# Kernel optimization log

Hardware: AMD Instinct MI355X
Metric: run time of the kernel (lower is better)

Reference implementation:

```python
import jax, jax.numpy as jnp
import numpy as np
from jax import lax

# program token ids
PAD, START, END, SCENE, INTERSECT, FILT, RELATE, QUERY = range(8)
SKIP = (PAD, START, END)


def conv2d(x, w, b, dil=1):
    # 'same' padding for odd kernels (3x3 pad=dil, 1x1 pad=0), NCHW/OIHW
    pad = dil * (w.shape[2] // 2)
    y = lax.conv_general_dilated(x, w, (1, 1), [(pad, pad), (pad, pad)],
                                 rhs_dilation=(dil, dil),
                                 dimension_numbers=('NCHW', 'OIHW', 'NCHW'))
    return y + b[None, :, None, None]


def maxpool2(x):
    return lax.reduce_window(x, -jnp.inf, lax.max, (1, 1, 2, 2), (1, 1, 2, 2), 'VALID')


def exec_program(prog, feat_input, p):
    """Run one (concrete) program over a batch of stem features. prog: tuple of ints,
    executed in reversed order exactly like TbDNet.forward."""
    B, _, H, W = feat_input.shape
    output = feat_input
    saved = None
    for t in reversed(prog):
        if t in SKIP:
            continue
        if t == SCENE:
            saved = output
            output = jnp.ones((B, 1, H, W), feat_input.dtype)
        elif t == INTERSECT:  # AndModule: elementwise min of attentions
            output = jnp.minimum(output, saved)
        elif t == FILT:
            a = feat_input * output  # [B,D,H,W] * [B,1,H,W]
            a = jax.nn.relu(conv2d(a, p['att_w1'], p['att_b1']))
            a = jax.nn.relu(conv2d(a, p['att_w2'], p['att_b2']))
            output = jax.nn.sigmoid(conv2d(a, p['att_w3'], p['att_b3']))
        elif t == RELATE:  # RelateModule: dilated conv stack (1,2,4,8,1) -> conv1x1 sigmoid
            a = feat_input * output
            for w, b, d in ((p['rel_w1'], p['rel_b1'], 1), (p['rel_w2'], p['rel_b2'], 2),
                            (p['rel_w3'], p['rel_b3'], 4), (p['rel_w4'], p['rel_b4'], 8),
                            (p['rel_w5'], p['rel_b5'], 1)):
                a = jax.nn.relu(conv2d(a, w, b, d))
            output = jax.nn.sigmoid(conv2d(a, p['rel_w6'], p['rel_b6']))
        elif t == QUERY:
            a = feat_input * output
            a = jax.nn.relu(conv2d(a, p['qry_w1'], p['qry_b1']))
            output = jax.nn.relu(conv2d(a, p['qry_w2'], p['qry_b2']))
    return output


def tbd_forward(feats, programs_np, p):
    B = feats.shape[0]
    stem = jax.nn.relu(conv2d(feats, p['stem_w1'], p['stem_b1']))
    stem = jax.nn.relu(conv2d(stem, p['stem_w2'], p['stem_b2']))  # [B,D,H,W]
    D, H, W = stem.shape[1], stem.shape[2], stem.shape[3]
    # group samples by identical program so dispatch runs batched, not per-sample
    groups = {}
    for n in range(B):
        groups.setdefault(tuple(int(v) for v in programs_np[n]), []).append(n)
    mod_out = jnp.zeros((B, D, H, W), feats.dtype)
    for prog, idxs in groups.items():
        idx = jnp.array(idxs)
        mod_out = mod_out.at[idx].set(exec_program(prog, stem[idx], p))
    # classifier: conv1x1 -> relu -> maxpool2 -> flatten -> fc -> relu -> fc
    x = jax.nn.relu(conv2d(mod_out, p['cls_w'], p['cls_b']))
    x = maxpool2(x)                        # [B,1024,7,7]
    x = x.reshape(B, -1)                   # [B,50176]
    x = jax.nn.relu(x @ p['fc1_w'].T + p['fc1_b'])
    return x @ p['fc2_w'].T + p['fc2_b']   # [B,28]


def setup_inputs() -> dict:
    key = jax.random.key(0)
    ks = iter(jax.random.split(key, 64))
    def rn(shape, s=0.05):
        return jax.random.normal(next(ks), shape, dtype=jnp.float32) * s
    B, Cin, H, W, D, P, L, A = 64, 1024, 14, 14, 128, 1024, 1024, 28
    feats = jax.random.normal(next(ks), (B, Cin, H, W), dtype=jnp.float32)
    # stored programs; execution order is reversed(stored)
    progA = [START, QUERY, FILT, RELATE, FILT, SCENE, END, PAD]            # scene->filter->relate->filter->query
    progB = [START, QUERY, INTERSECT, FILT, SCENE, FILT, SCENE, END]       # two filter branches -> intersect -> query
    programs = jnp.array([progA] * (B // 2) + [progB] * (B // 2), dtype=jnp.int32)
    inp = {'feats': feats, 'programs': programs,
           'stem_w1': rn((D, Cin, 3, 3), 0.02), 'stem_b1': rn((D,)),
           'stem_w2': rn((D, D, 3, 3)), 'stem_b2': rn((D,)),
           'att_w1': rn((D, D, 3, 3)), 'att_b1': rn((D,)),
           'att_w2': rn((D, D, 3, 3)), 'att_b2': rn((D,)),
           'att_w3': rn((1, D, 1, 1)), 'att_b3': rn((1,)),
           'rel_w1': rn((D, D, 3, 3)), 'rel_b1': rn((D,)),
           'rel_w2': rn((D, D, 3, 3)), 'rel_b2': rn((D,)),
           'rel_w3': rn((D, D, 3, 3)), 'rel_b3': rn((D,)),
           'rel_w4': rn((D, D, 3, 3)), 'rel_b4': rn((D,)),
           'rel_w5': rn((D, D, 3, 3)), 'rel_b5': rn((D,)),
           'rel_w6': rn((1, D, 1, 1)), 'rel_b6': rn((1,)),
           'qry_w1': rn((D, D, 3, 3)), 'qry_b1': rn((D,)),
           'qry_w2': rn((D, D, 3, 3)), 'qry_b2': rn((D,)),
           'cls_w': rn((P, D, 1, 1)), 'cls_b': rn((P,)),
           'fc1_w': rn((L, P * (H // 2) * (W // 2)), 0.01), 'fc1_b': rn((L,)),
           'fc2_w': rn((A, L)), 'fc2_b': rn((A,))}
    return inp


PARAM_NAMES = ['stem_w1', 'stem_b1', 'stem_w2', 'stem_b2',
               'att_w1', 'att_b1', 'att_w2', 'att_b2', 'att_w3', 'att_b3',
               'rel_w1', 'rel_b1', 'rel_w2', 'rel_b2', 'rel_w3', 'rel_b3',
               'rel_w4', 'rel_b4', 'rel_w5', 'rel_b5', 'rel_w6', 'rel_b6',
               'qry_w1', 'qry_b1', 'qry_w2', 'qry_b2',
               'cls_w', 'cls_b', 'fc1_w', 'fc1_b', 'fc2_w', 'fc2_b']


def reference(feats, programs, stem_w1, stem_b1, stem_w2, stem_b2,
              att_w1, att_b1, att_w2, att_b2, att_w3, att_b3,
              rel_w1, rel_b1, rel_w2, rel_b2, rel_w3, rel_b3,
              rel_w4, rel_b4, rel_w5, rel_b5, rel_w6, rel_b6,
              qry_w1, qry_b1, qry_w2, qry_b2,
              cls_w, cls_b, fc1_w, fc1_b, fc2_w, fc2_b):
    vals = [stem_w1, stem_b1, stem_w2, stem_b2,
            att_w1, att_b1, att_w2, att_b2, att_w3, att_b3,
            rel_w1, rel_b1, rel_w2, rel_b2, rel_w3, rel_b3,
            rel_w4, rel_b4, rel_w5, rel_b5, rel_w6, rel_b6,
            qry_w1, qry_b1, qry_w2, qry_b2,
            cls_w, cls_b, fc1_w, fc1_b, fc2_w, fc2_b]
    p = dict(zip(PARAM_NAMES, vals))
    return tbd_forward(feats, np.asarray(programs), p)
```

## Files before the change

kernel.cpp:

```cpp
#include <hip/hip_runtime.h>
#include <math.h>


typedef __attribute__((ext_vector_type(8)))  short   short8;
typedef __attribute__((ext_vector_type(8)))  __bf16  bf16x8;
typedef __attribute__((ext_vector_type(4)))  float   f32x4;

#define NROUNDS 11
#define NKS 98
#define S1KS 16

#define B_WSTEM1 0UL
#define B_WSTEM2 2359296UL
#define B_WMOD   2654208UL
#define B_WCLS   5308416UL
#define B_STEM   5570560UL
#define B_XA     8781824UL
#define B_XB     11993088UL
#define B_FEAT   15204352UL
#define B_ATTN   18415616UL
#define B_SAVED  18465792UL
#define B_SCHED  18515968UL
#define B_ACTB   18520064UL
#define B_FC1T   24942592UL
#define B_P1X1   25204736UL
#define B_S1P    67108864UL
#define B_FC1P   134217728UL

__device__ __forceinline__ unsigned short f2bf(float f) {
    __bf16 h = (__bf16)f;
    union { __bf16 h; unsigned short u; } c; c.h = h; return c.u;
}
__device__ __forceinline__ float bf2f(unsigned short u) {
    return __uint_as_float(((unsigned int)u) << 16);
}
__device__ __forceinline__ unsigned int pkbf(float a, float b) {
    return (unsigned int)f2bf(a) | ((unsigned int)f2bf(b) << 16);
}
__device__ __forceinline__ f32x4 mfma16(bf16x8 a, bf16x8 b, f32x4 c) {
    return __builtin_amdgcn_mfma_f32_16x16x32_bf16(a, b, c, 0, 0, 0);
}

struct PrepArgs { const float* src[12]; const int* prog; char* ws; };

__global__ __launch_bounds__(256) void k_prep(PrepArgs a)
{
    char* ws = a.ws;
    const int bx = blockIdx.x;
    if (bx < 768) {
        const int y = bx >> 6;
        const float* __restrict__ src = a.src[y];
        int gid = (bx & 63) * 256 + threadIdx.x;
        int gsz = 64 * 256;
        if (y == 11) {
            unsigned short* dst = (unsigned short*)(ws + B_WCLS);
            for (int i = gid; i < 131072; i += gsz) dst[i] = f2bf(src[i]);
        } else {
            const int IC = (y == 0) ? 1024 : 128;
            const int lg = (y == 0) ? 10 : 7;
            unsigned short* dst = (unsigned short*)(ws + ((y == 0) ? B_WSTEM1
                                        : (y == 1) ? B_WSTEM2
                                        : B_WMOD + (size_t)(y - 2) * 294912));
            const int total = 9 << (lg + 7);
            for (int i = gid; i < total; i += gsz) {
                int ic = i & (IC - 1);
                int oc = (i >> lg) & 127;
                int t  = i >> (lg + 7);
                dst[i] = f2bf(src[((size_t)oc * IC + ic) * 9 + t]);
            }
        }
        return;
    }
    int gid = (bx - 768) * 256 + threadIdx.x;
    int gsz = 256 * 256;
    float* attn  = (float*)(ws + B_ATTN);
    float* saved = (float*)(ws + B_SAVED);
    float* p1    = (float*)(ws + B_P1X1);
    for (int i = gid; i < 64 * 196; i += gsz) { attn[i] = 1.0f; saved[i] = 1.0f; }
    for (int i = gid; i < 8 * 64 * 196; i += gsz) p1[i] = 0.0f;
    unsigned int* fz = (unsigned int*)(ws + B_FEAT);
    for (int i = gid; i < 64 * 25088 / 2; i += gsz) fz[i] = 0u;
    if (gid < 64) {
        int n = gid;
        const int* prog = a.prog;
        int ent[NROUNDS];
        for (int r = 0; r < NROUNDS; ++r) ent[r] = 0;
        int rc = 0, nslot = 0;
        int pscene = 0, pinter = 0, pmat = 0, pmw = 0;
#define PREBITS ((pscene<<17)|(pinter<<18)|(pmat<<19)|(pmw<<22))
#define CLRPRE  (pscene = pinter = pmat = pmw = 0)
#define EMIT(v) do { if (rc < NROUNDS) ent[rc++] = (v); } while (0)
        for (int j = 7; j >= 0; --j) {
            int t = prog[n * 8 + j];
            switch (t) {
                case 3: pscene = 1; break;
                case 4: pinter = 1; break;
                case 5: {
                    int e1 = 3 | (0<<4) | (1<<8) | (1<<12) | (2<<13) | (0<<15) | PREBITS;
                    CLRPRE; EMIT(e1);
                    EMIT(3 | (1<<4) | (1<<8) | (0<<12) | (0<<13) | (1<<15)
                           | (1<<23) | (0<<24) | (nslot<<25));
                    pmat = nslot + 1; pmw = 0; nslot++;
                    break;
                }
                case 6: {
                    int e1 = 3 | (2<<4) | (1<<8) | (1<<12) | (2<<13) | (0<<15) | PREBITS;
                    CLRPRE; EMIT(e1);
                    EMIT(3 | (3<<4) | (2<<8) | (0<<12) | (0<<13) | (1<<15));
                    EMIT(3 | (4<<4) | (4<<8) | (0<<12) | (1<<13) | (0<<15));
                    EMIT(3 | (5<<4) | (8<<8) | (0<<12) | (0<<13) | (1<<15));
                    EMIT(3 | (6<<4) | (1<<8) | (0<<12) | (1<<13) | (0<<15)
                           | (1<<23) | (1<<24) | (nslot<<25));
                    pmat = nslot + 1; pmw = 1; nslot++;
                    break;
                }
                case 7: {
                    int e1 = 3 | (7<<4) | (1<<8) | (1<<12) | (2<<13) | (0<<15) | PREBITS;
                    CLRPRE; EMIT(e1);
                    EMIT(3 | (8<<4) | (1<<8) | (0<<12) | (0<<13) | (2<<15));
                    break;
                }
                default: break;
            }
        }
#undef EMIT
#undef PREBITS
#undef CLRPRE
        int* sched = (int*)(ws + B_SCHED);
        for (int r = 0; r < NROUNDS; ++r) sched[n * NROUNDS + r] = ent[r];
    }
}

__global__ __launch_bounds__(512) void k_stem1p(const float* __restrict__ feats,
                                                const unsigned short* __restrict__ wrep,
                                                char* ws)
{
    __shared__ unsigned short s_img[197 * 72];
    const int bx = blockIdx.x;
    const int n = bx >> 4, ks = bx & 15;
    const int tid = threadIdx.x, lane = tid & 63;
    const int w = tid >> 6, wm = w & 1, wn = w >> 1;
    const int l15 = lane & 15, lq = lane >> 4;

    if (tid < 36) ((unsigned int*)(s_img + 196 * 72))[tid] = 0u;

    int pglob[4], pbyt[4], pyv[4], pxv[4];
#pragma unroll
    for (int j = 0; j < 4; ++j) {
        int p  = (wn + 4 * j) * 16 + l15;
        pglob[j] = p;
        int py = p / 14;
        pyv[j] = (p < 196) ? py : 10000;
        pxv[j] = p - py * 14;
        pbyt[j] = p * 144 + lq * 16;
    }
    const int zaddr = 196 * 144 + lq * 16;
    const int nJ = (wn == 0) ? 4 : 3;

    f32x4 acc[4][4];
#pragma unroll
    for (int m = 0; m < 4; ++m)
#pragma unroll
        for (int j = 0; j < 4; ++j) acc[m][j] = (f32x4){0.f, 0.f, 0.f, 0.f};

    const int icg = tid & 15;
    const int qq0 = tid >> 4;
    const int icb = ks * 64;

    const float* sf = feats + ((size_t)n * 1024 + icb) * 196;
    for (int qq = qq0; qq < 49; qq += 32) {
        const float* p0 = sf + icg * 4 * 196 + qq * 4;
        float4 r0 = *(const float4*)(p0);
        float4 r1 = *(const float4*)(p0 + 196);
        float4 r2 = *(const float4*)(p0 + 392);
        float4 r3 = *(const float4*)(p0 + 588);
#pragma unroll
        for (int e = 0; e < 4; ++e) {
            uint2 v;
            v.x = pkbf(((const float*)&r0)[e], ((const float*)&r1)[e]);
            v.y = pkbf(((const float*)&r2)[e], ((const float*)&r3)[e]);
            *(uint2*)(s_img + (qq * 4 + e) * 72 + icg * 4) = v;
        }
    }
    __syncthreads();

#pragma unroll
    for (int t = 0; t < 9; ++t) {
        const int dy = t / 3 - 1, dx = t % 3 - 1;
        int baddr[4];
#pragma unroll
        for (int j = 0; j < 4; ++j) {
            int yy = pyv[j] + dy, xx = pxv[j] + dx;
            bool ok = ((unsigned)yy < 14u) && ((unsigned)xx < 14u);
            baddr[j] = ok ? (pbyt[j] + (dy * 14 + dx) * 144) : zaddr;
        }
#pragma unroll
        for (int kc = 0; kc < 2; ++kc) {
            const unsigned short* wt = wrep +
                ((size_t)(t * 128 + wm * 64 + l15) * 1024 + icb + kc * 32 + lq * 8);
            bf16x8 am[4];
#pragma unroll
            for (int m = 0; m < 4; ++m)
                am[m] = *(const bf16x8*)(wt + (size_t)m * 16 * 1024);
#pragma unroll
            for (int j = 0; j < 4; ++j) {
                if (j < nJ) {
                    bf16x8 b = *(const bf16x8*)((const char*)s_img + baddr[j] + kc * 64);
#pragma unroll
                    for (int m = 0; m < 4; ++m)
                        acc[m][j] = mfma16(am[m], b, acc[m][j]);
                }
            }
        }
    }

    unsigned short* part = (unsigned short*)(ws + B_S1P);
#pragma unroll
    for (int m = 0; m < 4; ++m) {
        const int oc = wm * 64 + m * 16 + lq * 4;
#pragma unroll
        for (int j = 0; j < 4; ++j) {
            if (j < nJ) {
                int p = pglob[j];
                if (p < 196) {
                    uint2 pk;
                    pk.x = pkbf(acc[m][j][0], acc[m][j][1]);
                    pk.y = pkbf(acc[m][j][2], acc[m][j][3]);
                    *(uint2*)(part + (((size_t)ks * 64 + n) * 196 + p) * 128 + oc) = pk;
                }
            }
        }
    }
}

__global__ __launch_bounds__(256) void k_stem1r(const char* __restrict__ ws_c,
                                                const float* __restrict__ bias,
                                                unsigned short* __restrict__ xa)
{
    int i = blockIdx.x * 256 + threadIdx.x;
    const unsigned short* part = (const unsigned short*)(ws_c + B_S1P);
    int oc8 = (i & 15) * 8;
    int np  = i >> 4;
    float s[8] = {};
#pragma unroll
    for (int ks = 0; ks < S1KS; ++ks) {
        short8 v = *(const short8*)(part + (((size_t)ks * 64) * 196 + np) * 128 + oc8);
#pragma unroll
        for (int e = 0; e < 8; ++e) s[e] += bf2f((unsigned short)v[e]);
    }
    short8 o;
#pragma unroll
    for (int e = 0; e < 8; ++e)
        o[e] = (short)f2bf(fmaxf(s[e] + bias[oc8 + e], 0.f));
    *(short8*)(xa + (size_t)np * 128 + oc8) = o;
}

__device__ void conv_core32(const unsigned short* __restrict__ srcB,
                            const float* __restrict__ s_gate,
                            const unsigned short* __restrict__ wrep,
                            const float* __restrict__ bias,
                            unsigned short* __restrict__ dst,
                            int dil, int oct, int pxh,
                            unsigned short* s_img,
                            int post, const float* __restrict__ pwv,
                            float* __restrict__ pdst)
{
    const int tid  = threadIdx.x, lane = tid & 63;
    const int w    = tid >> 6, wm = w & 1, wn = w >> 1;
    const int l15  = lane & 15, lq = lane >> 4;

    if (tid < 68) ((unsigned int*)s_img)[196 * 68 + tid] = 0u;

    int pglob[4], pbyt[4], pyv[4], pxv[4];
#pragma unroll
    for (int j = 0; j < 4; ++j) {
        int nt = wn + 2 * j;
        int p  = (pxh * 7 + nt) * 16 + l15;
        pglob[j] = p;
        int py = p / 14;
        pyv[j] = (p < 196) ? py : 10000;
        pxv[j] = p - py * 14;
        pbyt[j] = p * 272 + lq * 16;
    }
    const int zaddr = 196 * 272 + lq * 16;
    const int nNT = (wn == 0) ? 4 : 3;

    f32x4 acc[4];
#pragma unroll
    for (int j = 0; j < 4; ++j) acc[j] = (f32x4){0.f, 0.f, 0.f, 0.f};

    if (s_gate) {
        for (int i = tid; i < 196 * 16; i += 256) {
            int p = i >> 4, c8 = (i & 15) * 8;
            short8 v = *(const short8*)(srcB + p * 128 + c8);
            float g = s_gate[p];
            uint2 o0, o1;
            o0.x = pkbf(bf2f((unsigned short)v[0]) * g, bf2f((unsigned short)v[1]) * g);
            o0.y = pkbf(bf2f((unsigned short)v[2]) * g, bf2f((unsigned short)v[3]) * g);
            o1.x = pkbf(bf2f((unsigned short)v[4]) * g, bf2f((unsigned short)v[5]) * g);
            o1.y = pkbf(bf2f((unsigned short)v[6]) * g, bf2f((unsigned short)v[7]) * g);
            *(uint2*)(s_img + p * 136 + c8)     = o0;
            *(uint2*)(s_img + p * 136 + c8 + 4) = o1;
        }
    } else {
        for (int i = tid; i < 196 * 16; i += 256) {
            int p = i >> 4, c8 = (i & 15) * 8;
            *(short8*)(s_img + p * 136 + c8) = *(const short8*)(srcB + p * 128 + c8);
        }
    }
    __syncthreads();

    const unsigned short* wlane = wrep + (size_t)(oct * 32 + wm * 16 + l15) * 128 + lq * 8;
#pragma unroll
    for (int t = 0; t < 9; ++t) {
        const int dy = (t / 3 - 1) * dil, dx = (t % 3 - 1) * dil;
        int baddr[4];
#pragma unroll
        for (int j = 0; j < 4; ++j) {
            int yy = pyv[j] + dy, xx = pxv[j] + dx;
            bool ok = ((unsigned)yy < 14u) && ((unsigned)xx < 14u);
            baddr[j] = ok ? (pbyt[j] + (dy * 14 + dx) * 272) : zaddr;
        }
        const unsigned short* wt = wlane + (size_t)(t * 128) * 128;
#pragma unroll
        for (int kc = 0; kc < 4; ++kc) {
            bf16x8 a0 = *(const bf16x8*)(wt + kc * 32);
#pragma unroll
            for (int j = 0; j < 4; ++j) {
                if (j < nNT) {
                    bf16x8 b = *(const bf16x8*)((const char*)s_img + baddr[j] + kc * 64);
                    acc[j] = mfma16(a0, b, acc[j]);
                }
            }
        }
    }

    const int oc = oct * 32 + wm * 16 + lq * 4;
    const float4 b4 = *(const float4*)(bias + oc);
    float4 wv4;
    if (post) wv4 = *(const float4*)(pwv + oc);
#pragma unroll
    for (int j = 0; j < 4; ++j) {
        if (j < nNT) {
            int p = pglob[j];
            if (p < 196) {
                float v0 = fmaxf(acc[j][0] + b4.x, 0.f);
                float v1 = fmaxf(acc[j][1] + b4.y, 0.f);
                float v2 = fmaxf(acc[j][2] + b4.z, 0.f);
                float v3 = fmaxf(acc[j][3] + b4.w, 0.f);
                uint2 pk;
                pk.x = pkbf(v0, v1);
                pk.y = pkbf(v2, v3);
                *(uint2*)(dst + p * 128 + oc) = pk;
                if (post) {
                    float s = v0 * wv4.x + v1 * wv4.y + v2 * wv4.z + v3 * wv4.w;
                    atomicAdd(pdst + p, s);
                }
            }
        }
    }
}

__global__ __launch_bounds__(256) void k_conv_stem2(const unsigned short* __restrict__ srcBall,
                                                    const unsigned short* __restrict__ wrep,
                                                    const float* __restrict__ bias,
                                                    unsigned short* __restrict__ dstall)
{
    __shared__ unsigned short s_img[197 * 136];
    const int n = blockIdx.x >> 3, oct = (blockIdx.x >> 1) & 3, pxh = blockIdx.x & 1;
    conv_core32(srcBall + (size_t)n * 25088, nullptr, wrep, bias,
                dstall + (size_t)n * 25088, 1, oct, pxh, s_img, 0, nullptr, nullptr);
}

struct RArgs {
    char* ws;
    const float* mbias[9];
    const float* w1x1[2];
    const float* b1x1[2];
};

__global__ __launch_bounds__(256) void k_round(RArgs a, int r)
{
    __shared__ unsigned short s_img[197 * 136];
    __shared__ float s_gate[196];
    const int bx = blockIdx.x;
    const int n = bx >> 3, oct = (bx >> 1) & 3, pxh = bx & 1;
    char* ws = a.ws;
    const int* sched = (const int*)(ws + B_SCHED);
    const int e = sched[n * NROUNDS + r];
    if ((e & 15) == 0) return;
    const int tid = threadIdx.x;
    const int wset = (e >> 4) & 15, dil = (e >> 8) & 15, gatef = (e >> 12) & 1;
    const int srcid = (e >> 13) & 3, dstid = (e >> 15) & 3;
    const int fscene = (e >> 17) & 1, finter = (e >> 18) & 1;
    const int mslot = (e >> 19) & 7, mw = (e >> 22) & 1;
    const int post = (e >> 23) & 1, pw = (e >> 24) & 1, pslot = (e >> 25) & 7;

    float* attn  = (float*)(ws + B_ATTN)  + n * 196;
    float* saved = (float*)(ws + B_SAVED) + n * 196;
    float* p1    = (float*)(ws + B_P1X1);

    if (gatef) {
        if (tid < 196) {
            float cur = attn[tid];
            if (mslot) {
                float pv = p1[(size_t)(mslot - 1) * 12544 + n * 196 + tid];
                cur = 1.0f / (1.0f + __expf(-(pv + a.b1x1[mw][0])));
            }
            if (fscene) { saved[tid] = cur; cur = 1.0f; }
            if (finter) { cur = fminf(cur, saved[tid]); }
            if (mslot | fscene | finter) attn[tid] = cur;
            s_gate[tid] = cur;
        }
        __syncthreads();
    }

    const unsigned short* src = (const unsigned short*)(ws +
            (srcid == 2 ? B_STEM : srcid == 1 ? B_XB : B_XA)) + (size_t)n * 25088;
    unsigned short* dst = (unsigned short*)(ws +
            (dstid == 2 ? B_FEAT : dstid == 1 ? B_XB : B_XA)) + (size_t)n * 25088;
    const unsigned short* wrep = (const unsigned short*)(ws + B_WMOD) + (size_t)wset * 9 * 128 * 128;

    conv_core32(src, gatef ? s_gate : nullptr, wrep, a.mbias[wset], dst,
                dil, oct, pxh, s_img,
                post, post ? a.w1x1[pw] : nullptr,
                post ? (p1 + (size_t)pslot * 12544 + n * 196) : nullptr);
}

__global__ __launch_bounds__(256) void k_cls_pool(const unsigned short* __restrict__ featall,
                                                  const unsigned short* __restrict__ clsw,
                                                  const float* __restrict__ clsb,
                                                  unsigned short* __restrict__ actB)
{
    __shared__ char smem[197 * 272 + 64 * 200 * 4];
    unsigned short* s_img = (unsigned short*)smem;
    float* s_pool = (float*)(smem + 197 * 272);
    const int n = blockIdx.x >> 4, pt = blockIdx.x & 15;
    const int tid = threadIdx.x, lane = tid & 63, w = tid >> 6;
    const int l15 = lane & 15, lq = lane >> 4;
    const unsigned short* feat = featall + (size_t)n * 25088;

    if (tid < 68) ((unsigned int*)s_img)[196 * 68 + tid] = 0u;
    for (int i = tid; i < 196 * 16; i += 256) {
        int p = i >> 4, c8 = (i & 15) * 8;
        *(short8*)(s_img + p * 136 + c8) = *(const short8*)(feat + p * 128 + c8);
    }
    f32x4 acc[14];
#pragma unroll
    for (int j = 0; j < 14; ++j) acc[j] = (f32x4){0.f, 0.f, 0.f, 0.f};
    __syncthreads();

    const unsigned short* wl = clsw + (size_t)(pt * 64 + w * 16 + l15) * 128 + lq * 8;
#pragma unroll
    for (int kc = 0; kc < 4; ++kc) {
        bf16x8 a0 = *(const bf16x8*)(wl + kc * 32);
#pragma unroll
        for (int j = 0; j < 14; ++j) {
            int p = j * 16 + l15;
            int ba = (p < 196) ? (p * 272 + lq * 16 + kc * 64) : (196 * 272 + lq * 16);
            bf16x8 b = *(const bf16x8*)((const char*)s_img + ba);
            acc[j] = mfma16(a0, b, acc[j]);
        }
    }
    const int oc = pt * 64 + w * 16 + lq * 4;
    const float4 b4 = *(const float4*)(clsb + oc);
    const int pl = w * 16 + lq * 4;
#pragma unroll
    for (int j = 0; j < 14; ++j) {
        int p = j * 16 + l15;
        if (p < 196) {
            s_pool[(pl + 0) * 200 + p] = fmaxf(acc[j][0] + b4.x, 0.f);
            s_pool[(pl + 1) * 200 + p] = fmaxf(acc[j][1] + b4.y, 0.f);
            s_pool[(pl + 2) * 200 + p] = fmaxf(acc[j][2] + b4.z, 0.f);
            s_pool[(pl + 3) * 200 + p] = fmaxf(acc[j][3] + b4.w, 0.f);
        }
    }
    __syncthreads();
    for (int i = tid; i < 64 * 49; i += 256) {
        int plx = i / 49, q = i - plx * 49;
        int py = q / 7, qx = q - py * 7;
        const float* rp = s_pool + plx * 200 + py * 28 + qx * 2;
        float m = fmaxf(fmaxf(rp[0], rp[1]), fmaxf(rp[14], rp[15]));
        int k = (pt * 64 + plx) * 49 + q;
        int kb = k >> 6, lq2 = (k >> 4) & 3, hi = (k >> 3) & 1, e = k & 7;
        actB[((((size_t)kb * 4 + lq2) * 2 + hi) * 64 + n) * 8 + e] = f2bf(m);
    }
}

__global__ __launch_bounds__(256) void k_fc1p(const unsigned short* __restrict__ actB,
                                              const float* __restrict__ w,
                                              float* __restrict__ part)
{
    __shared__ unsigned short s_w[64 * 264];
    const int jt = blockIdx.x & 15, ks = blockIdx.x >> 4;
    const int tid = threadIdx.x, lane = tid & 63, wv = tid >> 6;
    const int l15 = lane & 15, lq = lane >> 4;
    const int k0 = ks * 512;

    f32x4 acc[4];
#pragma unroll
    for (int t = 0; t < 4; ++t) acc[t] = (f32x4){0.f, 0.f, 0.f, 0.f};

    float4 pf[16];

#define FC1_LOAD(ss_) do {                                                        \
    _Pragma("unroll")                                                             \
    for (int pass = 0; pass < 16; ++pass) {                                       \
        const int row_ = pass * 4 + wv;                                           \
        pf[pass] = *(const float4*)(w + (size_t)(jt * 64 + row_) * 50176 + k0     \
                                      + (ss_) * 256 + lane * 4);                  \
    } } while (0)

    FC1_LOAD(0);

    for (int ss = 0; ss < 2; ++ss) {
        __syncthreads();
#pragma unroll
        for (int pass = 0; pass < 16; ++pass) {
            const int row = pass * 4 + wv;
            uint2 v;
            v.x = pkbf(pf[pass].x, pf[pass].y);
            v.y = pkbf(pf[pass].z, pf[pass].w);
            *(uint2*)(s_w + row * 264 + lane * 4) = v;
        }
        __syncthreads();
        if (ss < 1) FC1_LOAD(1);

        const unsigned short* arow = s_w + (wv * 16 + l15) * 264;
#pragma unroll
        for (int kk = 0; kk < 8; ++kk) {
            bf16x8 a = *(const bf16x8*)(arow + kk * 32 + lq * 8);
            const int kglob = k0 + ss * 256 + kk * 32 + lq * 8;
            const int kb = kglob >> 6, lq2 = (kglob >> 4) & 3, hi = (kglob >> 3) & 1;
            const unsigned short* bp = actB +
                ((((size_t)kb * 4 + lq2) * 2 + hi) * 64 + l15) * 8;
#pragma unroll
            for (int t = 0; t < 4; ++t) {
                bf16x8 b = *(const bf16x8*)(bp + t * 128);
                acc[t] = mfma16(a, b, acc[t]);
            }
        }
    }
#undef FC1_LOAD

    float* pbase = part + ((size_t)ks * 1024 + jt * 64 + wv * 16 + lq * 4) * 64 + l15;
#pragma unroll
    for (int t = 0; t < 4; ++t)
#pragma unroll
        for (int r = 0; r < 4; ++r)
            pbase[(size_t)r * 64 + t * 16] = acc[t][r];
}

__global__ __launch_bounds__(256) void k_fc1r(const float* __restrict__ part,
                                              const float* __restrict__ b,
                                              float* __restrict__ fc1T)
{
    int i = blockIdx.x * 256 + threadIdx.x;
    if (i >= 65536) return;
    float s = 0.0f;
    for (int ks = 0; ks < NKS; ++ks) s += part[(size_t)ks * 65536 + i];
    int j = i >> 6;
    fc1T[i] = fmaxf(s + b[j], 0.0f);
}

__global__ __launch_bounds__(256) void k_fc2(const float* __restrict__ fc1T,
                                             const float* __restrict__ w,
                                             const float* __restrict__ b,
                                             float* __restrict__ out)
{
    __shared__ float red[256];
    const int a_ = blockIdx.x;
    const int tid = threadIdx.x, lane = tid & 63, q = tid >> 6;
    float acc = 0.0f;
    const float* wr = w + (size_t)a_ * 1024;
    for (int k = q * 256; k < q * 256 + 256; ++k)
        acc = fmaf(fc1T[k * 64 + lane], wr[k], acc);
    red[tid] = acc;
    __syncthreads();
    if (q == 0) {
        float s = red[tid] + red[tid + 64] + red[tid + 128] + red[tid + 192] + b[a_];
        out[lane * 28 + a_] = s;
    }
}

extern "C" void kernel_launch(void* const* d_in, const int* in_sizes, int n_in,
                              void* d_out, int out_size, void* d_ws, size_t ws_size,
                              hipStream_t stream)
{
    const float* feats = (const float*)d_in[0];
    const int*   prog  = (const int*)d_in[1];
    char* ws  = (char*)d_ws;
    float* out = (float*)d_out;

    PrepArgs pa;
    pa.src[0]  = (const float*)d_in[2];
    pa.src[1]  = (const float*)d_in[4];
    pa.src[2]  = (const float*)d_in[6];
    pa.src[3]  = (const float*)d_in[8];
    pa.src[4]  = (const float*)d_in[12];
    pa.src[5]  = (const float*)d_in[14];
    pa.src[6]  = (const float*)d_in[16];
    pa.src[7]  = (const float*)d_in[18];
    pa.src[8]  = (const float*)d_in[20];
    pa.src[9]  = (const float*)d_in[24];
    pa.src[10] = (const float*)d_in[26];
    pa.src[11] = (const float*)d_in[28];
    pa.prog = prog;
    pa.ws = ws;
    k_prep<<<1024, 256, 0, stream>>>(pa);

    k_stem1p<<<1024, 512, 0, stream>>>(feats, (const unsigned short*)(ws + B_WSTEM1), ws);
    k_stem1r<<<784, 256, 0, stream>>>(ws, (const float*)d_in[3],
                                      (unsigned short*)(ws + B_XA));

    k_conv_stem2<<<512, 256, 0, stream>>>((const unsigned short*)(ws + B_XA),
                                          (const unsigned short*)(ws + B_WSTEM2),
                                          (const float*)d_in[5],
                                          (unsigned short*)(ws + B_STEM));

    RArgs ga;
    ga.ws = ws;
    ga.mbias[0] = (const float*)d_in[7];
    ga.mbias[1] = (const float*)d_in[9];
    ga.mbias[2] = (const float*)d_in[13];
    ga.mbias[3] = (const float*)d_in[15];
    ga.mbias[4] = (const float*)d_in[17];
    ga.mbias[5] = (const float*)d_in[19];
    ga.mbias[6] = (const float*)d_in[21];
    ga.mbias[7] = (const float*)d_in[25];
    ga.mbias[8] = (const float*)d_in[27];
    ga.w1x1[0]  = (const float*)d_in[10];
    ga.w1x1[1]  = (const float*)d_in[22];
    ga.b1x1[0]  = (const float*)d_in[11];
    ga.b1x1[1]  = (const float*)d_in[23];

    for (int r = 0; r < NROUNDS; ++r)
        k_round<<<512, 256, 0, stream>>>(ga, r);

    k_cls_pool<<<1024, 256, 0, stream>>>((const unsigned short*)(ws + B_FEAT),
                                         (const unsigned short*)(ws + B_WCLS),
                                         (const float*)d_in[29],
                                         (unsigned short*)(ws + B_ACTB));
    k_fc1p<<<1568, 256, 0, stream>>>((const unsigned short*)(ws + B_ACTB),
                                     (const float*)d_in[30], (float*)(ws + B_FC1P));
    k_fc1r<<<256, 256, 0, stream>>>((const float*)(ws + B_FC1P), (const float*)d_in[31],
                                    (float*)(ws + B_FC1T));
    k_fc2<<<28, 256, 0, stream>>>((const float*)(ws + B_FC1T), (const float*)d_in[32],
                                  (const float*)d_in[33], out);
}
```

Measured before the change: 514.7 us.

## Fuse module conv chains per sample and fold stem reduce into stem2

Replaces the per-conv round launches with one launch per module slot, where a block runs a whole module's conv chain for one sample and keeps intermediates in shared memory. The stem1 partial reduction is merged into the stem2 kernel, and stem1 now reads a pre-transposed bf16 feature layout built in the prep kernel with a larger split-K chunk. This cuts launches and global round trips of intermediates. In exchange, the module kernel runs only 128 blocks and most do one-block-per-sample serial work, which reduces parallelism, and each thread holds 13 accumulators.

```diff
diff --git a/kernel.cpp b/kernel.cpp
--- a/kernel.cpp
+++ b/kernel.cpp
@@ -6,17 +6,15 @@
 typedef __attribute__((ext_vector_type(8)))  __bf16  bf16x8;
 typedef __attribute__((ext_vector_type(4)))  float   f32x4;
 
-#define NROUNDS 11
+#define NSLOTS 4
 #define NKS 98
-#define S1KS 16
+#define S1KS 8
 
 #define B_WSTEM1 0UL
 #define B_WSTEM2 2359296UL
 #define B_WMOD   2654208UL
 #define B_WCLS   5308416UL
 #define B_STEM   5570560UL
-#define B_XA     8781824UL
-#define B_XB     11993088UL
 #define B_FEAT   15204352UL
 #define B_ATTN   18415616UL
 #define B_SAVED  18465792UL
@@ -24,6 +22,7 @@
 #define B_ACTB   18520064UL
 #define B_FC1T   24942592UL
 #define B_P1X1   25204736UL
+#define B_FT     33554432UL
 #define B_S1P    67108864UL
 #define B_FC1P   134217728UL
 
@@ -41,12 +40,36 @@
     return __builtin_amdgcn_mfma_f32_16x16x32_bf16(a, b, c, 0, 0, 0);
 }
 
-struct PrepArgs { const float* src[12]; const int* prog; char* ws; };
+struct PrepArgs { const float* src[12]; const int* prog; const float* feats; char* ws; };
 
 __global__ __launch_bounds__(256) void k_prep(PrepArgs a)
 {
     char* ws = a.ws;
     const int bx = blockIdx.x;
+    if (bx >= 1024) {
+        __shared__ float s[32 * 201];
+        const int bx2 = bx - 1024;
+        const int n = bx2 >> 5, it = bx2 & 31;
+        const int tid = threadIdx.x, lane = tid & 63, w = tid >> 6;
+        const float* src = a.feats + ((size_t)n * 1024 + it * 32) * 196;
+        for (int r = w; r < 32; r += 4) {
+            if (lane < 49) {
+                float4 v = *(const float4*)(src + r * 196 + lane * 4);
+                float* sr = s + r * 201 + lane * 4;
+                sr[0] = v.x; sr[1] = v.y; sr[2] = v.z; sr[3] = v.w;
+            }
+        }
+        __syncthreads();
+        const int ic4 = (tid & 7) * 4;
+        unsigned short* dst = (unsigned short*)(ws + B_FT) + (size_t)n * 200704 + it * 32 + ic4;
+        for (int p = tid >> 3; p < 196; p += 32) {
+            uint2 v;
+            v.x = pkbf(s[(ic4 + 0) * 201 + p], s[(ic4 + 1) * 201 + p]);
+            v.y = pkbf(s[(ic4 + 2) * 201 + p], s[(ic4 + 3) * 201 + p]);
+            *(uint2*)(dst + (size_t)p * 1024) = v;
+        }
+        return;
+    }
     if (bx < 768) {
         const int y = bx >> 6;
         const float* __restrict__ src = a.src[y];
@@ -83,41 +106,33 @@
     if (gid < 64) {
         int n = gid;
         const int* prog = a.prog;
-        int ent[NROUNDS];
-        for (int r = 0; r < NROUNDS; ++r) ent[r] = 0;
+        int ent[NSLOTS];
+        for (int r = 0; r < NSLOTS; ++r) ent[r] = 0;
         int rc = 0, nslot = 0;
         int pscene = 0, pinter = 0, pmat = 0, pmw = 0;
 #define PREBITS ((pscene<<17)|(pinter<<18)|(pmat<<19)|(pmw<<22))
 #define CLRPRE  (pscene = pinter = pmat = pmw = 0)
-#define EMIT(v) do { if (rc < NROUNDS) ent[rc++] = (v); } while (0)
+#define EMIT(v) do { if (rc < NSLOTS) ent[rc++] = (v); } while (0)
         for (int j = 7; j >= 0; --j) {
             int t = prog[n * 8 + j];
             switch (t) {
                 case 3: pscene = 1; break;
                 case 4: pinter = 1; break;
                 case 5: {
-                    int e1 = 3 | (0<<4) | (1<<8) | (1<<12) | (2<<13) | (0<<15) | PREBITS;
+                    int e1 = 1 | (0 << 4) | PREBITS | (0 << 24) | (nslot << 25);
                     CLRPRE; EMIT(e1);
-                    EMIT(3 | (1<<4) | (1<<8) | (0<<12) | (0<<13) | (1<<15)
-                           | (1<<23) | (0<<24) | (nslot<<25));
                     pmat = nslot + 1; pmw = 0; nslot++;
                     break;
                 }
                 case 6: {
-                    int e1 = 3 | (2<<4) | (1<<8) | (1<<12) | (2<<13) | (0<<15) | PREBITS;
+                    int e1 = 2 | (2 << 4) | PREBITS | (1 << 24) | (nslot << 25);
                     CLRPRE; EMIT(e1);
-                    EMIT(3 | (3<<4) | (2<<8) | (0<<12) | (0<<13) | (1<<15));
-                    EMIT(3 | (4<<4) | (4<<8) | (0<<12) | (1<<13) | (0<<15));
-                    EMIT(3 | (5<<4) | (8<<8) | (0<<12) | (0<<13) | (1<<15));
-                    EMIT(3 | (6<<4) | (1<<8) | (0<<12) | (1<<13) | (0<<15)
-                           | (1<<23) | (1<<24) | (nslot<<25));
                     pmat = nslot + 1; pmw = 1; nslot++;
                     break;
                 }
                 case 7: {
-                    int e1 = 3 | (7<<4) | (1<<8) | (1<<12) | (2<<13) | (0<<15) | PREBITS;
+                    int e1 = 3 | (7 << 4) | PREBITS;
                     CLRPRE; EMIT(e1);
-                    EMIT(3 | (8<<4) | (1<<8) | (0<<12) | (0<<13) | (2<<15));
                     break;
                 }
                 default: break;
@@ -127,22 +142,29 @@
 #undef PREBITS
 #undef CLRPRE
         int* sched = (int*)(ws + B_SCHED);
-        for (int r = 0; r < NROUNDS; ++r) sched[n * NROUNDS + r] = ent[r];
-    }
-}
-
-__global__ __launch_bounds__(512) void k_stem1p(const float* __restrict__ feats,
+        for (int r = 0; r < NSLOTS; ++r) sched[n * NSLOTS + r] = ent[r];
+    }
+}
+
+__global__ __launch_bounds__(512) void k_stem1p(const unsigned short* __restrict__ ft,
                                                 const unsigned short* __restrict__ wrep,
                                                 char* ws)
 {
-    __shared__ unsigned short s_img[197 * 72];
+    __shared__ unsigned short s_img[197 * 136];
     const int bx = blockIdx.x;
-    const int n = bx >> 4, ks = bx & 15;
+    const int n = bx >> 3, ks = bx & 7;
     const int tid = threadIdx.x, lane = tid & 63;
     const int w = tid >> 6, wm = w & 1, wn = w >> 1;
     const int l15 = lane & 15, lq = lane >> 4;
-
-    if (tid < 36) ((unsigned int*)(s_img + 196 * 72))[tid] = 0u;
+    const int icb = ks * 128;
+
+    if (tid < 68) ((unsigned int*)s_img)[196 * 68 + tid] = 0u;
+
+    const unsigned short* slab = ft + (size_t)n * 200704 + icb;
+    for (int i = tid; i < 196 * 16; i += 512) {
+        int p = i >> 4, c8 = (i & 15) * 8;
+        *(short8*)(s_img + p * 136 + c8) = *(const short8*)(slab + (size_t)p * 1024 + c8);
+    }
 
     int pglob[4], pbyt[4], pyv[4], pxv[4];
 #pragma unroll
@@ -152,9 +174,9 @@
         int py = p / 14;
         pyv[j] = (p < 196) ? py : 10000;
         pxv[j] = p - py * 14;
-        pbyt[j] = p * 144 + lq * 16;
-    }
-    const int zaddr = 196 * 144 + lq * 16;
+        pbyt[j] = p * 272 + lq * 16;
+    }
+    const int zaddr = 196 * 272 + lq * 16;
     const int nJ = (wn == 0) ? 4 : 3;
 
     f32x4 acc[4][4];
@@ -162,26 +184,6 @@
     for (int m = 0; m < 4; ++m)
 #pragma unroll
         for (int j = 0; j < 4; ++j) acc[m][j] = (f32x4){0.f, 0.f, 0.f, 0.f};
-
-    const int icg = tid & 15;
-    const int qq0 = tid >> 4;
-    const int icb = ks * 64;
-
-    const float* sf = feats + ((size_t)n * 1024 + icb) * 196;
-    for (int qq = qq0; qq < 49; qq += 32) {
-        const float* p0 = sf + icg * 4 * 196 + qq * 4;
-        float4 r0 = *(const float4*)(p0);
-        float4 r1 = *(const float4*)(p0 + 196);
-        float4 r2 = *(const float4*)(p0 + 392);
-        float4 r3 = *(const float4*)(p0 + 588);
-#pragma unroll
-        for (int e = 0; e < 4; ++e) {
-            uint2 v;
-            v.x = pkbf(((const float*)&r0)[e], ((const float*)&r1)[e]);
-            v.y = pkbf(((const float*)&r2)[e], ((const float*)&r3)[e]);
-            *(uint2*)(s_img + (qq * 4 + e) * 72 + icg * 4) = v;
-        }
-    }
     __syncthreads();
 
 #pragma unroll
@@ -192,10 +194,10 @@
         for (int j = 0; j < 4; ++j) {
             int yy = pyv[j] + dy, xx = pxv[j] + dx;
             bool ok = ((unsigned)yy < 14u) && ((unsigned)xx < 14u);
-            baddr[j] = ok ? (pbyt[j] + (dy * 14 + dx) * 144) : zaddr;
-        }
-#pragma unroll
-        for (int kc = 0; kc < 2; ++kc) {
+            baddr[j] = ok ? (pbyt[j] + (dy * 14 + dx) * 272) : zaddr;
+        }
+#pragma unroll
+        for (int kc = 0; kc < 4; ++kc) {
             const unsigned short* wt = wrep +
                 ((size_t)(t * 128 + wm * 64 + l15) * 1024 + icb + kc * 32 + lq * 8);
             bf16x8 am[4];
@@ -233,49 +235,42 @@
     }
 }
 
-__global__ __launch_bounds__(256) void k_stem1r(const char* __restrict__ ws_c,
-                                                const float* __restrict__ bias,
-                                                unsigned short* __restrict__ xa)
-{
-    int i = blockIdx.x * 256 + threadIdx.x;
-    const unsigned short* part = (const unsigned short*)(ws_c + B_S1P);
-    int oc8 = (i & 15) * 8;
-    int np  = i >> 4;
-    float s[8] = {};
-#pragma unroll
-    for (int ks = 0; ks < S1KS; ++ks) {
-        short8 v = *(const short8*)(part + (((size_t)ks * 64) * 196 + np) * 128 + oc8);
-#pragma unroll
-        for (int e = 0; e < 8; ++e) s[e] += bf2f((unsigned short)v[e]);
-    }
-    short8 o;
-#pragma unroll
-    for (int e = 0; e < 8; ++e)
-        o[e] = (short)f2bf(fmaxf(s[e] + bias[oc8 + e], 0.f));
-    *(short8*)(xa + (size_t)np * 128 + oc8) = o;
-}
-
-__device__ void conv_core32(const unsigned short* __restrict__ srcB,
-                            const float* __restrict__ s_gate,
-                            const unsigned short* __restrict__ wrep,
-                            const float* __restrict__ bias,
-                            unsigned short* __restrict__ dst,
-                            int dil, int oct, int pxh,
-                            unsigned short* s_img,
-                            int post, const float* __restrict__ pwv,
-                            float* __restrict__ pdst)
-{
-    const int tid  = threadIdx.x, lane = tid & 63;
-    const int w    = tid >> 6, wm = w & 1, wn = w >> 1;
-    const int l15  = lane & 15, lq = lane >> 4;
+__global__ __launch_bounds__(512) void k_stem2f(char* ws,
+                                                const float* __restrict__ bias1,
+                                                const unsigned short* __restrict__ wrep,
+                                                const float* __restrict__ bias2,
+                                                unsigned short* __restrict__ stem)
+{
+    __shared__ unsigned short s_img[197 * 136];
+    const int n = blockIdx.x >> 2, oct = blockIdx.x & 3;
+    const int tid = threadIdx.x, lane = tid & 63;
+    const int w = tid >> 6, wo = w & 1, wn = w >> 1;
+    const int l15 = lane & 15, lq = lane >> 4;
 
     if (tid < 68) ((unsigned int*)s_img)[196 * 68 + tid] = 0u;
 
+    const unsigned short* part = (const unsigned short*)(ws + B_S1P);
+    for (int i = tid; i < 196 * 16; i += 512) {
+        int p = i >> 4, c8 = (i & 15) * 8;
+        float s[8] = {};
+#pragma unroll
+        for (int ks = 0; ks < S1KS; ++ks) {
+            short8 v = *(const short8*)(part + (((size_t)ks * 64 + n) * 196 + p) * 128 + c8);
+#pragma unroll
+            for (int e = 0; e < 8; ++e) s[e] += bf2f((unsigned short)v[e]);
+        }
+        short8 o;
+#pragma unroll
+        for (int e = 0; e < 8; ++e)
+            o[e] = (short)f2bf(fmaxf(s[e] + bias1[c8 + e], 0.f));
+        *(short8*)(s_img + p * 136 + c8) = o;
+    }
+    __syncthreads();
+
     int pglob[4], pbyt[4], pyv[4], pxv[4];
 #pragma unroll
     for (int j = 0; j < 4; ++j) {
-        int nt = wn + 2 * j;
-        int p  = (pxh * 7 + nt) * 16 + l15;
+        int p  = (wn + 4 * j) * 16 + l15;
         pglob[j] = p;
         int py = p / 14;
         pyv[j] = (p < 196) ? py : 10000;
@@ -283,43 +278,21 @@
         pbyt[j] = p * 272 + lq * 16;
     }
     const int zaddr = 196 * 272 + lq * 16;
-    const int nNT = (wn == 0) ? 4 : 3;
 
     f32x4 acc[4];
 #pragma unroll
     for (int j = 0; j < 4; ++j) acc[j] = (f32x4){0.f, 0.f, 0.f, 0.f};
 
-    if (s_gate) {
-        for (int i = tid; i < 196 * 16; i += 256) {
-            int p = i >> 4, c8 = (i & 15) * 8;
-            short8 v = *(const short8*)(srcB + p * 128 + c8);
-            float g = s_gate[p];
-            uint2 o0, o1;
-            o0.x = pkbf(bf2f((unsigned short)v[0]) * g, bf2f((unsigned short)v[1]) * g);
-            o0.y = pkbf(bf2f((unsigned short)v[2]) * g, bf2f((unsigned short)v[3]) * g);
-            o1.x = pkbf(bf2f((unsigned short)v[4]) * g, bf2f((unsigned short)v[5]) * g);
-            o1.y = pkbf(bf2f((unsigned short)v[6]) * g, bf2f((unsigned short)v[7]) * g);
-            *(uint2*)(s_img + p * 136 + c8)     = o0;
-            *(uint2*)(s_img + p * 136 + c8 + 4) = o1;
-        }
-    } else {
-        for (int i = tid; i < 196 * 16; i += 256) {
-            int p = i >> 4, c8 = (i & 15) * 8;
-            *(short8*)(s_img + p * 136 + c8) = *(const short8*)(srcB + p * 128 + c8);
-        }
-    }
-    __syncthreads();
-
-    const unsigned short* wlane = wrep + (size_t)(oct * 32 + wm * 16 + l15) * 128 + lq * 8;
+    const unsigned short* wlane = wrep + (size_t)(oct * 32 + wo * 16 + l15) * 128 + lq * 8;
 #pragma unroll
     for (int t = 0; t < 9; ++t) {
-        const int dy = (t / 3 - 1) * dil, dx = (t % 3 - 1) * dil;
-        int baddr[4];
+        const int dy = t / 3 - 1, dx = t % 3 - 1;
+        int ba[4];
 #pragma unroll
         for (int j = 0; j < 4; ++j) {
             int yy = pyv[j] + dy, xx = pxv[j] + dx;
             bool ok = ((unsigned)yy < 14u) && ((unsigned)xx < 14u);
-            baddr[j] = ok ? (pbyt[j] + (dy * 14 + dx) * 272) : zaddr;
+            ba[j] = ok ? (pbyt[j] + (dy * 14 + dx) * 272) : zaddr;
         }
         const unsigned short* wt = wlane + (size_t)(t * 128) * 128;
 #pragma unroll
@@ -327,49 +300,25 @@
             bf16x8 a0 = *(const bf16x8*)(wt + kc * 32);
 #pragma unroll
             for (int j = 0; j < 4; ++j) {
-                if (j < nNT) {
-                    bf16x8 b = *(const bf16x8*)((const char*)s_img + baddr[j] + kc * 64);
-                    acc[j] = mfma16(a0, b, acc[j]);
-                }
-            }
-        }
-    }
-
-    const int oc = oct * 32 + wm * 16 + lq * 4;
-    const float4 b4 = *(const float4*)(bias + oc);
-    float4 wv4;
-    if (post) wv4 = *(const float4*)(pwv + oc);
+                bf16x8 b = *(const bf16x8*)((const char*)s_img + ba[j] + kc * 64);
+                acc[j] = mfma16(a0, b, acc[j]);
+            }
+        }
+    }
+
+    const int oc = oct * 32 + wo * 16 + lq * 4;
+    const float4 b4 = *(const float4*)(bias2 + oc);
+    unsigned short* dst = stem + (size_t)n * 25088;
 #pragma unroll
     for (int j = 0; j < 4; ++j) {
-        if (j < nNT) {
-            int p = pglob[j];
-            if (p < 196) {
-                float v0 = fmaxf(acc[j][0] + b4.x, 0.f);
-                float v1 = fmaxf(acc[j][1] + b4.y, 0.f);
-                float v2 = fmaxf(acc[j][2] + b4.z, 0.f);
-                float v3 = fmaxf(acc[j][3] + b4.w, 0.f);
-                uint2 pk;
-                pk.x = pkbf(v0, v1);
-                pk.y = pkbf(v2, v3);
-                *(uint2*)(dst + p * 128 + oc) = pk;
-                if (post) {
-                    float s = v0 * wv4.x + v1 * wv4.y + v2 * wv4.z + v3 * wv4.w;
-                    atomicAdd(pdst + p, s);
-                }
-            }
-        }
-    }
-}
-
-__global__ __launch_bounds__(256) void k_conv_stem2(const unsigned short* __restrict__ srcBall,
-                                                    const unsigned short* __restrict__ wrep,
-                                                    const float* __restrict__ bias,
-                                                    unsigned short* __restrict__ dstall)
-{
-    __shared__ unsigned short s_img[197 * 136];
-    const int n = blockIdx.x >> 3, oct = (blockIdx.x >> 1) & 3, pxh = blockIdx.x & 1;
-    conv_core32(srcBall + (size_t)n * 25088, nullptr, wrep, bias,
-                dstall + (size_t)n * 25088, 1, oct, pxh, s_img, 0, nullptr, nullptr);
+        int p = pglob[j];
+        if (p < 196) {
+            uint2 pk;
+            pk.x = pkbf(fmaxf(acc[j][0] + b4.x, 0.f), fmaxf(acc[j][1] + b4.y, 0.f));
+            pk.y = pkbf(fmaxf(acc[j][2] + b4.z, 0.f), fmaxf(acc[j][3] + b4.w, 0.f));
+            *(uint2*)(dst + p * 128 + oc) = pk;
+        }
+    }
 }
 
 struct RArgs {
@@ -379,52 +328,158 @@
     const float* b1x1[2];
 };
 
-__global__ __launch_bounds__(256) void k_round(RArgs a, int r)
+__global__ __launch_bounds__(512) void k_mod(RArgs a, int r)
 {
     __shared__ unsigned short s_img[197 * 136];
     __shared__ float s_gate[196];
+    __shared__ float s_post[196];
     const int bx = blockIdx.x;
-    const int n = bx >> 3, oct = (bx >> 1) & 3, pxh = bx & 1;
+    const int n = bx >> 1, half = bx & 1;
     char* ws = a.ws;
     const int* sched = (const int*)(ws + B_SCHED);
-    const int e = sched[n * NROUNDS + r];
-    if ((e & 15) == 0) return;
-    const int tid = threadIdx.x;
-    const int wset = (e >> 4) & 15, dil = (e >> 8) & 15, gatef = (e >> 12) & 1;
-    const int srcid = (e >> 13) & 3, dstid = (e >> 15) & 3;
+    const int e = sched[n * NSLOTS + r];
+    const int op = e & 3;
+    if (op == 0) return;
+    if (op != 3 && half) return;
+
+    const int tid = threadIdx.x, lane = tid & 63, w = tid >> 6;
+    const int l15 = lane & 15, lq = lane >> 4;
+    const int ws1 = (e >> 4) & 15;
     const int fscene = (e >> 17) & 1, finter = (e >> 18) & 1;
     const int mslot = (e >> 19) & 7, mw = (e >> 22) & 1;
-    const int post = (e >> 23) & 1, pw = (e >> 24) & 1, pslot = (e >> 25) & 7;
+    const int pw = (e >> 24) & 1, pslot = (e >> 25) & 7;
 
     float* attn  = (float*)(ws + B_ATTN)  + n * 196;
     float* saved = (float*)(ws + B_SAVED) + n * 196;
     float* p1    = (float*)(ws + B_P1X1);
 
-    if (gatef) {
-        if (tid < 196) {
-            float cur = attn[tid];
-            if (mslot) {
-                float pv = p1[(size_t)(mslot - 1) * 12544 + n * 196 + tid];
-                cur = 1.0f / (1.0f + __expf(-(pv + a.b1x1[mw][0])));
-            }
-            if (fscene) { saved[tid] = cur; cur = 1.0f; }
-            if (finter) { cur = fminf(cur, saved[tid]); }
-            if (mslot | fscene | finter) attn[tid] = cur;
-            s_gate[tid] = cur;
-        }
+    if (tid < 68) ((unsigned int*)s_img)[196 * 68 + tid] = 0u;
+    if (tid < 196) {
+        s_post[tid] = 0.f;
+        float cur = attn[tid];
+        if (mslot) {
+            float pv = p1[(size_t)(mslot - 1) * 12544 + n * 196 + tid];
+            cur = 1.0f / (1.0f + __expf(-(pv + a.b1x1[mw][0])));
+        }
+        if (fscene) { saved[tid] = cur; cur = 1.0f; }
+        if (finter) { cur = fminf(cur, saved[tid]); }
+        if (mslot | fscene | finter) attn[tid] = cur;
+        s_gate[tid] = cur;
+    }
+    __syncthreads();
+
+    const unsigned short* stem = (const unsigned short*)(ws + B_STEM) + (size_t)n * 25088;
+    for (int i = tid; i < 196 * 16; i += 512) {
+        int p = i >> 4, c8 = (i & 15) * 8;
+        short8 v = *(const short8*)(stem + p * 128 + c8);
+        float g = s_gate[p];
+        uint2 o0, o1;
+        o0.x = pkbf(bf2f((unsigned short)v[0]) * g, bf2f((unsigned short)v[1]) * g);
+        o0.y = pkbf(bf2f((unsigned short)v[2]) * g, bf2f((unsigned short)v[3]) * g);
+        o1.x = pkbf(bf2f((unsigned short)v[4]) * g, bf2f((unsigned short)v[5]) * g);
+        o1.y = pkbf(bf2f((unsigned short)v[6]) * g, bf2f((unsigned short)v[7]) * g);
+        *(uint2*)(s_img + p * 136 + c8)     = o0;
+        *(uint2*)(s_img + p * 136 + c8 + 4) = o1;
+    }
+
+    const unsigned short* wmod = (const unsigned short*)(ws + B_WMOD);
+    const int zaddr = 196 * 272 + lq * 16;
+    const int nconv = (op == 2) ? 5 : 2;
+
+    int pg2[13], pb2[13], pyv2[13], pxv2[13];
+#pragma unroll
+    for (int j2 = 0; j2 < 13; ++j2) {
+        int p = j2 * 16 + l15;
+        pg2[j2] = p;
+        int py = p / 14;
+        pyv2[j2] = (p < 196) ? py : 10000;
+        pxv2[j2] = p - py * 14;
+        pb2[j2] = p * 272 + lq * 16;
+    }
+
+    for (int c = 0; c < nconv; ++c) {
         __syncthreads();
-    }
-
-    const unsigned short* src = (const unsigned short*)(ws +
-            (srcid == 2 ? B_STEM : srcid == 1 ? B_XB : B_XA)) + (size_t)n * 25088;
-    unsigned short* dst = (unsigned short*)(ws +
-            (dstid == 2 ? B_FEAT : dstid == 1 ? B_XB : B_XA)) + (size_t)n * 25088;
-    const unsigned short* wrep = (const unsigned short*)(ws + B_WMOD) + (size_t)wset * 9 * 128 * 128;
-
-    conv_core32(src, gatef ? s_gate : nullptr, wrep, a.mbias[wset], dst,
-                dil, oct, pxh, s_img,
-                post, post ? a.w1x1[pw] : nullptr,
-                post ? (p1 + (size_t)pslot * 12544 + n * 196) : nullptr);
+        const int dil = (op == 2) ? ((c == 1) ? 2 : (c == 2) ? 4 : (c == 3) ? 8 : 1) : 1;
+        const unsigned short* wt0 = wmod + (size_t)(ws1 + c) * 147456;
+
+        f32x4 acc1[13];
+#pragma unroll
+        for (int j2 = 0; j2 < 13; ++j2) acc1[j2] = (f32x4){0.f, 0.f, 0.f, 0.f};
+
+#pragma unroll
+        for (int t = 0; t < 9; ++t) {
+            const int dy = (t / 3 - 1) * dil, dx = (t % 3 - 1) * dil;
+            int ba[13];
+#pragma unroll
+            for (int j2 = 0; j2 < 13; ++j2) {
+                int yy = pyv2[j2] + dy, xx = pxv2[j2] + dx;
+                bool ok = ((unsigned)yy < 14u) && ((unsigned)xx < 14u);
+                ba[j2] = ok ? (pb2[j2] + (dy * 14 + dx) * 272) : zaddr;
+            }
+#pragma unroll
+            for (int kc = 0; kc < 4; ++kc) {
+                bf16x8 av = *(const bf16x8*)(wt0 +
+                    (size_t)(t * 128 + w * 16 + l15) * 128 + kc * 32 + lq * 8);
+#pragma unroll
+                for (int j2 = 0; j2 < 13; ++j2) {
+                    bf16x8 b = *(const bf16x8*)((const char*)s_img + ba[j2] + kc * 64);
+                    acc1[j2] = mfma16(av, b, acc1[j2]);
+                }
+            }
+        }
+        __syncthreads();
+
+        const int oc1 = w * 16 + lq * 4;
+        const float4 b4 = *(const float4*)(a.mbias[ws1 + c] + oc1);
+
+        if (c < nconv - 1) {
+#pragma unroll
+            for (int j2 = 0; j2 < 13; ++j2) {
+                int p = pg2[j2];
+                if (p < 196) {
+                    uint2 pk;
+                    pk.x = pkbf(fmaxf(acc1[j2][0] + b4.x, 0.f),
+                                fmaxf(acc1[j2][1] + b4.y, 0.f));
+                    pk.y = pkbf(fmaxf(acc1[j2][2] + b4.z, 0.f),
+                                fmaxf(acc1[j2][3] + b4.w, 0.f));
+                    *(uint2*)(s_img + p * 136 + oc1) = pk;
+                }
+            }
+        } else if (op == 3) {
+            if ((w >> 2) == half) {
+                unsigned short* feat = (unsigned short*)(ws + B_FEAT) + (size_t)n * 25088;
+#pragma unroll
+                for (int j2 = 0; j2 < 13; ++j2) {
+                    int p = pg2[j2];
+                    if (p < 196) {
+                        uint2 pk;
+                        pk.x = pkbf(fmaxf(acc1[j2][0] + b4.x, 0.f),
+                                    fmaxf(acc1[j2][1] + b4.y, 0.f));
+                        pk.y = pkbf(fmaxf(acc1[j2][2] + b4.z, 0.f),
+                                    fmaxf(acc1[j2][3] + b4.w, 0.f));
+                        *(uint2*)(feat + p * 128 + oc1) = pk;
+                    }
+                }
+            }
+        } else {
+            const float4 wv4 = *(const float4*)(a.w1x1[pw] + oc1);
+#pragma unroll
+            for (int j2 = 0; j2 < 13; ++j2) {
+                int p = pg2[j2];
+                float v0 = fmaxf(acc1[j2][0] + b4.x, 0.f);
+                float v1 = fmaxf(acc1[j2][1] + b4.y, 0.f);
+                float v2 = fmaxf(acc1[j2][2] + b4.z, 0.f);
+                float v3 = fmaxf(acc1[j2][3] + b4.w, 0.f);
+                float s = v0 * wv4.x + v1 * wv4.y + v2 * wv4.z + v3 * wv4.w;
+                s += __shfl_xor(s, 16);
+                s += __shfl_xor(s, 32);
+                if (lq == 0 && p < 196) atomicAdd(&s_post[p], s);
+            }
+            __syncthreads();
+            if (tid < 196)
+                p1[(size_t)pslot * 12544 + n * 196 + tid] = s_post[tid];
+        }
+    }
 }
 
 __global__ __launch_bounds__(256) void k_cls_pool(const unsigned short* __restrict__ featall,
@@ -482,8 +537,8 @@
         const float* rp = s_pool + plx * 200 + py * 28 + qx * 2;
         float m = fmaxf(fmaxf(rp[0], rp[1]), fmaxf(rp[14], rp[15]));
         int k = (pt * 64 + plx) * 49 + q;
-        int kb = k >> 6, lq2 = (k >> 4) & 3, hi = (k >> 3) & 1, e = k & 7;
-        actB[((((size_t)kb * 4 + lq2) * 2 + hi) * 64 + n) * 8 + e] = f2bf(m);
+        int kb = k >> 6, lq2 = (k >> 4) & 3, hi = (k >> 3) & 1, e2 = k & 7;
+        actB[((((size_t)kb * 4 + lq2) * 2 + hi) * 64 + n) * 8 + e2] = f2bf(m);
     }
 }
 
@@ -547,8 +602,8 @@
 #pragma unroll
     for (int t = 0; t < 4; ++t)
 #pragma unroll
-        for (int r = 0; r < 4; ++r)
-            pbase[(size_t)r * 64 + t * 16] = acc[t][r];
+        for (int r2 = 0; r2 < 4; ++r2)
+            pbase[(size_t)r2 * 64 + t * 16] = acc[t][r2];
 }
 
 __global__ __launch_bounds__(256) void k_fc1r(const float* __restrict__ part,
@@ -606,17 +661,17 @@
     pa.src[10] = (const float*)d_in[26];
     pa.src[11] = (const float*)d_in[28];
     pa.prog = prog;
+    pa.feats = feats;
     pa.ws = ws;
-    k_prep<<<1024, 256, 0, stream>>>(pa);
-
-    k_stem1p<<<1024, 512, 0, stream>>>(feats, (const unsigned short*)(ws + B_WSTEM1), ws);
-    k_stem1r<<<784, 256, 0, stream>>>(ws, (const float*)d_in[3],
-                                      (unsigned short*)(ws + B_XA));
-
-    k_conv_stem2<<<512, 256, 0, stream>>>((const unsigned short*)(ws + B_XA),
-                                          (const unsigned short*)(ws + B_WSTEM2),
-                                          (const float*)d_in[5],
-                                          (unsigned short*)(ws + B_STEM));
+    k_prep<<<3072, 256, 0, stream>>>(pa);
+
+    k_stem1p<<<512, 512, 0, stream>>>((const unsigned short*)(ws + B_FT),
+                                      (const unsigned short*)(ws + B_WSTEM1), ws);
+
+    k_stem2f<<<256, 512, 0, stream>>>(ws, (const float*)d_in[3],
+                                      (const unsigned short*)(ws + B_WSTEM2),
+                                      (const float*)d_in[5],
+                                      (unsigned short*)(ws + B_STEM));
 
     RArgs ga;
     ga.ws = ws;
@@ -634,8 +689,8 @@
     ga.b1x1[0]  = (const float*)d_in[11];
     ga.b1x1[1]  = (const float*)d_in[23];
 
-    for (int r = 0; r < NROUNDS; ++r)
-        k_round<<<512, 256, 0, stream>>>(ga, r);
+    for (int r = 0; r < NSLOTS; ++r)
+        k_mod<<<128, 512, 0, stream>>>(ga, r);
 
     k_cls_pool<<<1024, 256, 0, stream>>>((const unsigned short*)(ws + B_FEAT),
                                          (const unsigned short*)(ws + B_WCLS),
```

Result: faster. 489.1 us (median of 3 runs) (-5.0%).
